# Kernel tuning notes

Measured on AMD Instinct MI355X. Metric: run time of the kernel, lower is better.

The kernel has to match this reference:

```python
import math
import jax, jax.numpy as jnp
import numpy as np

B, T, D = 4, 4096, 512


def setup_inputs() -> dict:
    key = jax.random.key(0)
    k1, _ = jax.random.split(key)
    x = jax.random.normal(k1, (B, T, D), dtype=jnp.float32)
    log_alpha = jnp.zeros((), dtype=jnp.float32)
    return {"x": x, "log_alpha": log_alpha}


def _gelu_tanh(x):
    c = math.sqrt(2.0 / math.pi)
    return 0.5 * x * (1.0 + jnp.tanh(c * (x + 0.044715 * x * x * x)))


def reference(x, log_alpha):
    Bx, Tx, Dx = x.shape
    alpha = jax.nn.softplus(log_alpha)
    # F.normalize(dim=-1): x / max(||x||, eps)
    norm = jnp.maximum(jnp.linalg.norm(x, axis=-1, keepdims=True), 1e-12)
    x_norm = x / norm
    sim = jnp.einsum("btd,bsd->bts", x_norm, x_norm)  # [B,T,T]
    # causal mask: triu incl. diagonal (col >= row) filled with -2.0
    row = jnp.arange(Tx)[:, None]
    col = jnp.arange(Tx)[None, :]
    mask = col >= row  # [T,T]
    sim = jnp.where(mask[None], jnp.float32(-2.0), sim)
    max_sim = jnp.max(sim, axis=-1)  # [B,T]
    max_sim = jnp.maximum(max_sim, -1.0)
    familiarity = (max_sim + 1.0) * 0.5
    novelty = 1.0 - familiarity
    gate = 1.0 + alpha * novelty[..., None]  # [B,T,1]
    return _gelu_tanh(x * gate)
```

## Files before the change

### kernel.cpp

```cpp
#include <hip/hip_runtime.h>
#include <hip/hip_bf16.h>
#include <math.h>

#define B_ 4
#define T_ 4096
#define D_ 512
#define BT 128
#define BK 64
#define STEPS (D_ / BK)
#define NT (T_ / BT)
#define NPAIR (NT * (NT + 1) / 2)


typedef float f32x4 __attribute__((ext_vector_type(4)));
typedef long i64x2 __attribute__((ext_vector_type(2)));

__device__ __forceinline__ unsigned f2ord(float f) {
    unsigned u = __float_as_uint(f);
    return (u & 0x80000000u) ? ~u : (u | 0x80000000u);
}
__device__ __forceinline__ float ord2f(unsigned u) {
    unsigned b = (u & 0x80000000u) ? (u ^ 0x80000000u) : ~u;
    return __uint_as_float(b);
}

__device__ __forceinline__ void async16(const unsigned char* g, unsigned char* l) {
    __builtin_amdgcn_global_load_lds(
        (const __attribute__((address_space(1))) unsigned int*)g,
        (__attribute__((address_space(3))) unsigned int*)l, 16, 0, 0);
}

__global__ __launch_bounds__(256) void k_norm(const float* __restrict__ x,
                                              unsigned char* __restrict__ xn,
                                              unsigned* __restrict__ maxsim) {
    int w = (blockIdx.x * 256 + threadIdx.x) >> 6;
    int l = threadIdx.x & 63;
    const float4* xr = (const float4*)(x + (size_t)w * D_);
    float4 a = xr[l];
    float4 b = xr[l + 64];
    float ss = a.x * a.x + a.y * a.y + a.z * a.z + a.w * a.w +
               b.x * b.x + b.y * b.y + b.z * b.z + b.w * b.w;
#pragma unroll
    for (int off = 32; off > 0; off >>= 1) ss += __shfl_xor(ss, off);
    float inv = 1.0f / fmaxf(sqrtf(ss), 1e-12f);
    int u0 = __builtin_amdgcn_cvt_pk_fp8_f32(a.x * inv, a.y * inv, 0, false);
    u0 = __builtin_amdgcn_cvt_pk_fp8_f32(a.z * inv, a.w * inv, u0, true);
    int u1 = __builtin_amdgcn_cvt_pk_fp8_f32(b.x * inv, b.y * inv, 0, false);
    u1 = __builtin_amdgcn_cvt_pk_fp8_f32(b.z * inv, b.w * inv, u1, true);
    unsigned* xo = (unsigned*)(xn + (size_t)w * D_);
    int off4 = (l >> 4) * 16 + ((l >> 1) & 3) * 4 + ((l >> 3) & 1) * 2 + (l & 1);
    xo[off4]      = (unsigned)u0;
    xo[off4 + 64] = (unsigned)u1;
    if (l == 0) maxsim[w] = f2ord(-2.0f);
}

__global__ __launch_bounds__(256) void k_maxsim(const unsigned char* __restrict__ xn,
                                                unsigned* __restrict__ maxsim) {
    __shared__ __align__(16) unsigned char Buf[3][16384];
    const int b = blockIdx.y;
    const int p = blockIdx.x;
    int ti = (int)((sqrtf(8.0f * (float)p + 1.0f) - 1.0f) * 0.5f);
    while ((ti + 1) * (ti + 2) / 2 <= p) ti++;
    while (ti * (ti + 1) / 2 > p) ti--;
    const int si = p - ti * (ti + 1) / 2;
    const int t0 = ti * BT, s0 = si * BT;

    const int tid = threadIdx.x;
    const int wave = tid >> 6, lane = tid & 63;
    const int wm = wave >> 1, wn = wave & 1;
    const int qa = lane >> 4, la = lane & 15;
    const int swz = (la >> 1) & 3;

    const unsigned char* Ab = xn + (size_t)(b * T_ + t0) * D_;
    const unsigned char* Bb = xn + (size_t)(b * T_ + s0) * D_;

    const int c0 = tid,       r0_ = c0 >> 2, g0 = (c0 & 3) ^ ((r0_ >> 1) & 3);
    const int c1 = 256 + tid, r1_ = c1 >> 2, g1 = (c1 & 3) ^ ((r1_ >> 1) & 3);
    const unsigned char* gA0 = Ab + (size_t)r0_ * D_ + g0 * 16;
    const unsigned char* gA1 = Ab + (size_t)r1_ * D_ + g1 * 16;
    const unsigned char* gB0 = Bb + (size_t)r0_ * D_ + g0 * 16;
    const unsigned char* gB1 = Bb + (size_t)r1_ * D_ + g1 * 16;
    const int ldsb0 = (wave * 64) * 16;
    const int ldsb1 = (256 + wave * 64) * 16;

#define STAGE(step, st)                                            \
    do {                                                           \
        async16(gA0 + (step) * BK, &Buf[st][ldsb0]);               \
        async16(gB0 + (step) * BK, &Buf[st][8192 + ldsb0]);        \
        async16(gA1 + (step) * BK, &Buf[st][ldsb1]);               \
        async16(gB1 + (step) * BK, &Buf[st][8192 + ldsb1]);        \
    } while (0)

    f32x4 acc[4][4];
#pragma unroll
    for (int i = 0; i < 4; i++)
#pragma unroll
        for (int j = 0; j < 4; j++) acc[i][j] = (f32x4){0.f, 0.f, 0.f, 0.f};

    const int rpos = (qa ^ swz) * 16;

    STAGE(0, 0);
    STAGE(1, 1);

#pragma unroll
    for (int k = 0; k < STEPS; ++k) {
        const int cur = k % 3;
        if (k == STEPS - 1) __builtin_amdgcn_s_waitcnt(0x0F70);
        else                __builtin_amdgcn_s_waitcnt(0x0F74);
        __builtin_amdgcn_s_barrier();
        __asm__ __volatile__("" ::: "memory");
        if (k + 2 < STEPS) STAGE(k + 2, (k + 2) % 3);

        const unsigned char* As = &Buf[cur][0];
        const unsigned char* Bs = &Buf[cur][8192];
        i64x2 af[4], bfr[4];
#pragma unroll
        for (int i = 0; i < 4; i++)
            af[i] = *(const i64x2*)&As[(wm * 64 + i * 16 + la) * 64 + rpos];
#pragma unroll
        for (int j = 0; j < 4; j++)
            bfr[j] = *(const i64x2*)&Bs[(wn * 64 + j * 16 + la) * 64 + rpos];
#pragma unroll
        for (int h = 0; h < 2; h++)
#pragma unroll
            for (int i = 0; i < 4; i++)
#pragma unroll
                for (int j = 0; j < 4; j++)
                    acc[i][j] = __builtin_amdgcn_mfma_f32_16x16x32_fp8_fp8(
                        af[i][h], bfr[j][h], acc[i][j], 0, 0, 0);
    }
#undef STAGE

    const bool diag = (ti == si);
#pragma unroll
    for (int i = 0; i < 4; i++) {
#pragma unroll
        for (int r = 0; r < 4; r++) {
            int tl = wm * 64 + i * 16 + qa * 4 + r;
            float m = -2.0f;
#pragma unroll
            for (int j = 0; j < 4; j++) {
                int sl = wn * 64 + j * 16 + la;
                float v = acc[i][j][r];
                if (!diag || sl < tl) m = fmaxf(m, v);
            }
#pragma unroll
            for (int off = 1; off < 16; off <<= 1) m = fmaxf(m, __shfl_xor(m, off));
            if (la == 0) atomicMax(&maxsim[b * T_ + t0 + tl], f2ord(m));
        }
    }
}

__device__ __forceinline__ float gelu_tanh(float y) {
    float t = tanhf(0.7978845608028654f * (y + 0.044715f * y * y * y));
    return 0.5f * y * (1.0f + t);
}

__global__ __launch_bounds__(256) void k_gate(const float* __restrict__ x,
                                              const float* __restrict__ log_alpha,
                                              const unsigned* __restrict__ maxsim,
                                              float* __restrict__ out) {
    int idx = blockIdx.x * 256 + threadIdx.x;
    float la = log_alpha[0];
    float alpha = (la > 20.0f) ? la : log1pf(expf(la));
    int row = idx >> 7;
    float m = fmaxf(ord2f(maxsim[row]), -1.0f);
    float novelty = 1.0f - (m + 1.0f) * 0.5f;
    float gate = 1.0f + alpha * novelty;
    float4 v = ((const float4*)x)[idx];
    float4 o;
    o.x = gelu_tanh(v.x * gate);
    o.y = gelu_tanh(v.y * gate);
    o.z = gelu_tanh(v.z * gate);
    o.w = gelu_tanh(v.w * gate);
    ((float4*)out)[idx] = o;
}

extern "C" void kernel_launch(void* const* d_in, const int* in_sizes, int n_in,
                              void* d_out, int out_size, void* d_ws, size_t ws_size,
                              hipStream_t stream) {
    const float* x = (const float*)d_in[0];
    const float* log_alpha = (const float*)d_in[1];
    float* out = (float*)d_out;

    unsigned* maxsim = (unsigned*)d_ws;
    unsigned char* xn = (unsigned char*)d_ws + 65536;

    const int rows = B_ * T_;
    k_norm<<<rows / 4, 256, 0, stream>>>(x, xn, maxsim);

    dim3 g2(NPAIR, B_);
    k_maxsim<<<g2, 256, 0, stream>>>(xn, maxsim);

    k_gate<<<(B_ * T_ * D_ / 4) / 256, 256, 0, stream>>>(x, log_alpha, maxsim, out);
}
```

Measured before the change: 131.3 us.

## Switch maxsim GEMM to 32x32x64 scaled FP8 MFMA with block-order remap

Replaces the 16x16x32 FP8 MFMA tiles with the gfx950 scaled 32x32x64 f8f6f4 MFMA and unit scales. This cuts the instruction count and the number of LDS fragment loads per K step. It drops the custom byte permutation in the normalization store and changes the LDS read addressing to match the new operand layout. It also remaps block indices so consecutive blocks are strided across the work list, likely to spread work across XCDs for better L2 locality. The new fragment layout and epilogue row mapping add correctness risk.

```diff
diff --git a/kernel.cpp b/kernel.cpp
--- a/kernel.cpp
+++ b/kernel.cpp
@@ -10,10 +10,13 @@
 #define STEPS (D_ / BK)
 #define NT (T_ / BT)
 #define NPAIR (NT * (NT + 1) / 2)
-
-
-typedef float f32x4 __attribute__((ext_vector_type(4)));
-typedef long i64x2 __attribute__((ext_vector_type(2)));
+#define NBLK (NPAIR * B_)
+#define SCL 0x7F7F7F7F
+
+
+typedef float f32x16 __attribute__((ext_vector_type(16)));
+typedef int v4i __attribute__((ext_vector_type(4)));
+typedef int v8i __attribute__((ext_vector_type(8)));
 
 __device__ __forceinline__ unsigned f2ord(float f) {
     unsigned u = __float_as_uint(f);
@@ -48,17 +51,18 @@
     int u1 = __builtin_amdgcn_cvt_pk_fp8_f32(b.x * inv, b.y * inv, 0, false);
     u1 = __builtin_amdgcn_cvt_pk_fp8_f32(b.z * inv, b.w * inv, u1, true);
     unsigned* xo = (unsigned*)(xn + (size_t)w * D_);
-    int off4 = (l >> 4) * 16 + ((l >> 1) & 3) * 4 + ((l >> 3) & 1) * 2 + (l & 1);
-    xo[off4]      = (unsigned)u0;
-    xo[off4 + 64] = (unsigned)u1;
+    xo[l]      = (unsigned)u0;
+    xo[l + 64] = (unsigned)u1;
     if (l == 0) maxsim[w] = f2ord(-2.0f);
 }
 
 __global__ __launch_bounds__(256) void k_maxsim(const unsigned char* __restrict__ xn,
                                                 unsigned* __restrict__ maxsim) {
     __shared__ __align__(16) unsigned char Buf[3][16384];
-    const int b = blockIdx.y;
-    const int p = blockIdx.x;
+    const int lin = blockIdx.x + NPAIR * blockIdx.y;
+    const int wrk = (lin & 7) * (NBLK / 8) + (lin >> 3);
+    const int b = wrk / NPAIR;
+    const int p = wrk - b * NPAIR;
     int ti = (int)((sqrtf(8.0f * (float)p + 1.0f) - 1.0f) * 0.5f);
     while ((ti + 1) * (ti + 2) / 2 <= p) ti++;
     while (ti * (ti + 1) / 2 > p) ti--;
@@ -68,8 +72,8 @@
     const int tid = threadIdx.x;
     const int wave = tid >> 6, lane = tid & 63;
     const int wm = wave >> 1, wn = wave & 1;
-    const int qa = lane >> 4, la = lane & 15;
-    const int swz = (la >> 1) & 3;
+    const int lr = lane & 31;
+    const int h  = lane >> 5;
 
     const unsigned char* Ab = xn + (size_t)(b * T_ + t0) * D_;
     const unsigned char* Bb = xn + (size_t)(b * T_ + s0) * D_;
@@ -91,13 +95,21 @@
         async16(gB1 + (step) * BK, &Buf[st][8192 + ldsb1]);        \
     } while (0)
 
-    f32x4 acc[4][4];
-#pragma unroll
-    for (int i = 0; i < 4; i++)
-#pragma unroll
-        for (int j = 0; j < 4; j++) acc[i][j] = (f32x4){0.f, 0.f, 0.f, 0.f};
-
-    const int rpos = (qa ^ swz) * 16;
+#define MFMA(Aop, Bop, C) \
+    __builtin_amdgcn_mfma_scale_f32_32x32x64_f8f6f4((Aop), (Bop), (C), 0, 0, 0, SCL, 0, SCL)
+
+    f32x16 acc[2][2];
+#pragma unroll
+    for (int i = 0; i < 2; i++)
+#pragma unroll
+        for (int j = 0; j < 2; j++)
+#pragma unroll
+            for (int r = 0; r < 16; r++) acc[i][j][r] = 0.0f;
+
+    const int s_ = (lr >> 1) & 3;
+    const int pb = ((2 * h) ^ s_) * 16;
+    const int offA = (wm * 64 + lr) * 64 + pb;
+    const int offB = 8192 + (wn * 64 + lr) * 64 + pb;
 
     STAGE(0, 0);
     STAGE(1, 1);
@@ -111,42 +123,45 @@
         __asm__ __volatile__("" ::: "memory");
         if (k + 2 < STEPS) STAGE(k + 2, (k + 2) % 3);
 
-        const unsigned char* As = &Buf[cur][0];
-        const unsigned char* Bs = &Buf[cur][8192];
-        i64x2 af[4], bfr[4];
-#pragma unroll
-        for (int i = 0; i < 4; i++)
-            af[i] = *(const i64x2*)&As[(wm * 64 + i * 16 + la) * 64 + rpos];
-#pragma unroll
-        for (int j = 0; j < 4; j++)
-            bfr[j] = *(const i64x2*)&Bs[(wn * 64 + j * 16 + la) * 64 + rpos];
-#pragma unroll
-        for (int h = 0; h < 2; h++)
-#pragma unroll
-            for (int i = 0; i < 4; i++)
-#pragma unroll
-                for (int j = 0; j < 4; j++)
-                    acc[i][j] = __builtin_amdgcn_mfma_f32_16x16x32_fp8_fp8(
-                        af[i][h], bfr[j][h], acc[i][j], 0, 0, 0);
+        const unsigned char* Bs = &Buf[cur][0];
+        v4i a0l = *(const v4i*)(Bs + offA);
+        v4i a0h = *(const v4i*)(Bs + (offA ^ 16));
+        v4i a1l = *(const v4i*)(Bs + offA + 2048);
+        v4i a1h = *(const v4i*)(Bs + (offA ^ 16) + 2048);
+        v4i b0l = *(const v4i*)(Bs + offB);
+        v4i b0h = *(const v4i*)(Bs + (offB ^ 16));
+        v4i b1l = *(const v4i*)(Bs + offB + 2048);
+        v4i b1h = *(const v4i*)(Bs + (offB ^ 16) + 2048);
+        const v8i A0 = __builtin_shufflevector(a0l, a0h, 0, 1, 2, 3, 4, 5, 6, 7);
+        const v8i A1 = __builtin_shufflevector(a1l, a1h, 0, 1, 2, 3, 4, 5, 6, 7);
+        const v8i B0 = __builtin_shufflevector(b0l, b0h, 0, 1, 2, 3, 4, 5, 6, 7);
+        const v8i B1 = __builtin_shufflevector(b1l, b1h, 0, 1, 2, 3, 4, 5, 6, 7);
+        acc[0][0] = MFMA(A0, B0, acc[0][0]);
+        acc[0][1] = MFMA(A0, B1, acc[0][1]);
+        acc[1][0] = MFMA(A1, B0, acc[1][0]);
+        acc[1][1] = MFMA(A1, B1, acc[1][1]);
     }
 #undef STAGE
+#undef MFMA
 
     const bool diag = (ti == si);
 #pragma unroll
-    for (int i = 0; i < 4; i++) {
-#pragma unroll
-        for (int r = 0; r < 4; r++) {
-            int tl = wm * 64 + i * 16 + qa * 4 + r;
+    for (int i = 0; i < 2; i++) {
+#pragma unroll
+        for (int reg = 0; reg < 16; reg++) {
+            const int tl = wm * 64 + i * 32 + (reg & 3) + 8 * (reg >> 2) + 4 * h;
             float m = -2.0f;
-#pragma unroll
-            for (int j = 0; j < 4; j++) {
-                int sl = wn * 64 + j * 16 + la;
-                float v = acc[i][j][r];
-                if (!diag || sl < tl) m = fmaxf(m, v);
+            {
+                const int sl0 = wn * 64 + lr;
+                float v0 = acc[i][0][reg];
+                if (!diag || sl0 < tl) m = fmaxf(m, v0);
+                const int sl1 = sl0 + 32;
+                float v1 = acc[i][1][reg];
+                if (!diag || sl1 < tl) m = fmaxf(m, v1);
             }
 #pragma unroll
-            for (int off = 1; off < 16; off <<= 1) m = fmaxf(m, __shfl_xor(m, off));
-            if (la == 0) atomicMax(&maxsim[b * T_ + t0 + tl], f2ord(m));
+            for (int off = 1; off < 32; off <<= 1) m = fmaxf(m, __shfl_xor(m, off));
+            if (lr == 0) atomicMax(&maxsim[b * T_ + t0 + tl], f2ord(m));
         }
     }
 }
```

After: 220.5 us. +68.0%, slower.

## Process two tile pairs per block with a continuous cross-tile load pipeline

Applied to the files above, without the earlier changes.

Each maxsim block now handles two consecutive (b, tile-pair) work items over 16 K-steps. The triple-buffered async LDS prefetch runs straight through the boundary between them, so the second tile's loads start during the first tile's compute. The first epilogue runs mid-loop at step 8. This halves the block count and removes one pipeline prologue and drain per tile. In exchange there is less parallelism (1056 blocks), a mid-loop epilogue that may stall the MFMA stream, and extra register pressure from holding two sets of coordinates.

```diff
diff --git a/kernel.cpp b/kernel.cpp
--- a/kernel.cpp
+++ b/kernel.cpp
@@ -10,6 +10,7 @@
 #define STEPS (D_ / BK)
 #define NT (T_ / BT)
 #define NPAIR (NT * (NT + 1) / 2)
+#define NBLK (NPAIR * B_)
 
 
 typedef float f32x4 __attribute__((ext_vector_type(4)));
@@ -57,13 +58,6 @@
 __global__ __launch_bounds__(256) void k_maxsim(const unsigned char* __restrict__ xn,
                                                 unsigned* __restrict__ maxsim) {
     __shared__ __align__(16) unsigned char Buf[3][16384];
-    const int b = blockIdx.y;
-    const int p = blockIdx.x;
-    int ti = (int)((sqrtf(8.0f * (float)p + 1.0f) - 1.0f) * 0.5f);
-    while ((ti + 1) * (ti + 2) / 2 <= p) ti++;
-    while (ti * (ti + 1) / 2 > p) ti--;
-    const int si = p - ti * (ti + 1) / 2;
-    const int t0 = ti * BT, s0 = si * BT;
 
     const int tid = threadIdx.x;
     const int wave = tid >> 6, lane = tid & 63;
@@ -71,24 +65,40 @@
     const int qa = lane >> 4, la = lane & 15;
     const int swz = (la >> 1) & 3;
 
-    const unsigned char* Ab = xn + (size_t)(b * T_ + t0) * D_;
-    const unsigned char* Bb = xn + (size_t)(b * T_ + s0) * D_;
-
     const int c0 = tid,       r0_ = c0 >> 2, g0 = (c0 & 3) ^ ((r0_ >> 1) & 3);
     const int c1 = 256 + tid, r1_ = c1 >> 2, g1 = (c1 & 3) ^ ((r1_ >> 1) & 3);
-    const unsigned char* gA0 = Ab + (size_t)r0_ * D_ + g0 * 16;
-    const unsigned char* gA1 = Ab + (size_t)r1_ * D_ + g1 * 16;
-    const unsigned char* gB0 = Bb + (size_t)r0_ * D_ + g0 * 16;
-    const unsigned char* gB1 = Bb + (size_t)r1_ * D_ + g1 * 16;
+    const size_t gofA0 = (size_t)r0_ * D_ + g0 * 16;
+    const size_t gofA1 = (size_t)r1_ * D_ + g1 * 16;
     const int ldsb0 = (wave * 64) * 16;
     const int ldsb1 = (256 + wave * 64) * 16;
 
-#define STAGE(step, st)                                            \
-    do {                                                           \
-        async16(gA0 + (step) * BK, &Buf[st][ldsb0]);               \
-        async16(gB0 + (step) * BK, &Buf[st][8192 + ldsb0]);        \
-        async16(gA1 + (step) * BK, &Buf[st][ldsb1]);               \
-        async16(gB1 + (step) * BK, &Buf[st][8192 + ldsb1]);        \
+    int bb[2], tt0[2], ss0[2];
+    bool dg[2];
+#pragma unroll
+    for (int q = 0; q < 2; q++) {
+        int w = blockIdx.x * 2 + q;
+        int b = w / NPAIR;
+        int p = w - b * NPAIR;
+        int ti = (int)((sqrtf(8.0f * (float)p + 1.0f) - 1.0f) * 0.5f);
+        while ((ti + 1) * (ti + 2) / 2 <= p) ti++;
+        while (ti * (ti + 1) / 2 > p) ti--;
+        int si = p - ti * (ti + 1) / 2;
+        bb[q] = b; tt0[q] = ti * BT; ss0[q] = si * BT; dg[q] = (ti == si);
+    }
+    const unsigned char* pA_0 = xn + (size_t)(bb[0] * T_ + tt0[0]) * D_;
+    const unsigned char* pB_0 = xn + (size_t)(bb[0] * T_ + ss0[0]) * D_;
+    const unsigned char* pA_1 = xn + (size_t)(bb[1] * T_ + tt0[1]) * D_;
+    const unsigned char* pB_1 = xn + (size_t)(bb[1] * T_ + ss0[1]) * D_;
+
+#define STAGE(g)                                                          \
+    do {                                                                  \
+        const unsigned char* _A = ((g) < 8) ? pA_0 : pA_1;                \
+        const unsigned char* _B = ((g) < 8) ? pB_0 : pB_1;                \
+        const int _o = ((g) & 7) * BK;                                    \
+        async16(_A + gofA0 + _o, &Buf[(g) % 3][ldsb0]);                   \
+        async16(_B + gofA0 + _o, &Buf[(g) % 3][8192 + ldsb0]);            \
+        async16(_A + gofA1 + _o, &Buf[(g) % 3][ldsb1]);                   \
+        async16(_B + gofA1 + _o, &Buf[(g) % 3][8192 + ldsb1]);            \
     } while (0)
 
     f32x4 acc[4][4];
@@ -97,19 +107,47 @@
 #pragma unroll
         for (int j = 0; j < 4; j++) acc[i][j] = (f32x4){0.f, 0.f, 0.f, 0.f};
 
+    auto epi = [&](int be, int t0e, bool diage) {
+#pragma unroll
+        for (int i = 0; i < 4; i++) {
+#pragma unroll
+            for (int r = 0; r < 4; r++) {
+                int tl = wm * 64 + i * 16 + qa * 4 + r;
+                float m = -2.0f;
+#pragma unroll
+                for (int j = 0; j < 4; j++) {
+                    int sl = wn * 64 + j * 16 + la;
+                    float v = acc[i][j][r];
+                    if (!diage || sl < tl) m = fmaxf(m, v);
+                }
+#pragma unroll
+                for (int off = 1; off < 16; off <<= 1) m = fmaxf(m, __shfl_xor(m, off));
+                if (la == 0) atomicMax(&maxsim[be * T_ + t0e + tl], f2ord(m));
+            }
+        }
+    };
+
     const int rpos = (qa ^ swz) * 16;
 
-    STAGE(0, 0);
-    STAGE(1, 1);
-
-#pragma unroll
-    for (int k = 0; k < STEPS; ++k) {
+    STAGE(0);
+    STAGE(1);
+
+#pragma unroll
+    for (int k = 0; k < 16; ++k) {
         const int cur = k % 3;
-        if (k == STEPS - 1) __builtin_amdgcn_s_waitcnt(0x0F70);
-        else                __builtin_amdgcn_s_waitcnt(0x0F74);
+        if (k == 15) __builtin_amdgcn_s_waitcnt(0x0F70);
+        else         __builtin_amdgcn_s_waitcnt(0x0F74);
         __builtin_amdgcn_s_barrier();
         __asm__ __volatile__("" ::: "memory");
-        if (k + 2 < STEPS) STAGE(k + 2, (k + 2) % 3);
+        if (k + 2 < 16) STAGE(k + 2);
+
+        if (k == 8) {
+            epi(bb[0], tt0[0], dg[0]);
+#pragma unroll
+            for (int i = 0; i < 4; i++)
+#pragma unroll
+                for (int j = 0; j < 4; j++) acc[i][j] = (f32x4){0.f, 0.f, 0.f, 0.f};
+        }
 
         const unsigned char* As = &Buf[cur][0];
         const unsigned char* Bs = &Buf[cur][8192];
@@ -131,24 +169,7 @@
     }
 #undef STAGE
 
-    const bool diag = (ti == si);
-#pragma unroll
-    for (int i = 0; i < 4; i++) {
-#pragma unroll
-        for (int r = 0; r < 4; r++) {
-            int tl = wm * 64 + i * 16 + qa * 4 + r;
-            float m = -2.0f;
-#pragma unroll
-            for (int j = 0; j < 4; j++) {
-                int sl = wn * 64 + j * 16 + la;
-                float v = acc[i][j][r];
-                if (!diag || sl < tl) m = fmaxf(m, v);
-            }
-#pragma unroll
-            for (int off = 1; off < 16; off <<= 1) m = fmaxf(m, __shfl_xor(m, off));
-            if (la == 0) atomicMax(&maxsim[b * T_ + t0 + tl], f2ord(m));
-        }
-    }
+    epi(bb[1], tt0[1], dg[1]);
 }
 
 __device__ __forceinline__ float gelu_tanh(float y) {
@@ -189,8 +210,7 @@
     const int rows = B_ * T_;
     k_norm<<<rows / 4, 256, 0, stream>>>(x, xn, maxsim);
 
-    dim3 g2(NPAIR, B_);
-    k_maxsim<<<g2, 256, 0, stream>>>(xn, maxsim);
+    k_maxsim<<<NBLK / 2, 256, 0, stream>>>(xn, maxsim);
 
     k_gate<<<(B_ * T_ * D_ / 4) / 256, 256, 0, stream>>>(x, log_alpha, maxsim, out);
 }
```

After: 134.6 us. 2.5% more time.

## Give each wave private LDS staging to drop block barriers in maxsim GEMM

Applied to the files above, without the earlier changes.

Each wave now loads its own 64-row A and B slices into a private double-buffered LDS region instead of sharing a block-wide triple buffer. The per-step s_barrier is removed and replaced by a wait on the wave's own LDS reads before it reuses the buffer. This is meant to remove cross-wave synchronisation stalls. In exchange, tiles that were shared across waves are now loaded twice, so global/L2 traffic rises, and LDS use grows to 64KB, which can lower occupancy.

```diff
diff --git a/kernel.cpp b/kernel.cpp
--- a/kernel.cpp
+++ b/kernel.cpp
@@ -56,7 +56,7 @@
 
 __global__ __launch_bounds__(256) void k_maxsim(const unsigned char* __restrict__ xn,
                                                 unsigned* __restrict__ maxsim) {
-    __shared__ __align__(16) unsigned char Buf[3][16384];
+    __shared__ __align__(16) unsigned char Buf[4][2][8192];
     const int b = blockIdx.y;
     const int p = blockIdx.x;
     int ti = (int)((sqrtf(8.0f * (float)p + 1.0f) - 1.0f) * 0.5f);
@@ -71,24 +71,26 @@
     const int qa = lane >> 4, la = lane & 15;
     const int swz = (la >> 1) & 3;
 
-    const unsigned char* Ab = xn + (size_t)(b * T_ + t0) * D_;
-    const unsigned char* Bb = xn + (size_t)(b * T_ + s0) * D_;
-
-    const int c0 = tid,       r0_ = c0 >> 2, g0 = (c0 & 3) ^ ((r0_ >> 1) & 3);
-    const int c1 = 256 + tid, r1_ = c1 >> 2, g1 = (c1 & 3) ^ ((r1_ >> 1) & 3);
-    const unsigned char* gA0 = Ab + (size_t)r0_ * D_ + g0 * 16;
-    const unsigned char* gA1 = Ab + (size_t)r1_ * D_ + g1 * 16;
-    const unsigned char* gB0 = Bb + (size_t)r0_ * D_ + g0 * 16;
-    const unsigned char* gB1 = Bb + (size_t)r1_ * D_ + g1 * 16;
-    const int ldsb0 = (wave * 64) * 16;
-    const int ldsb1 = (256 + wave * 64) * 16;
-
-#define STAGE(step, st)                                            \
-    do {                                                           \
-        async16(gA0 + (step) * BK, &Buf[st][ldsb0]);               \
-        async16(gB0 + (step) * BK, &Buf[st][8192 + ldsb0]);        \
-        async16(gA1 + (step) * BK, &Buf[st][ldsb1]);               \
-        async16(gB1 + (step) * BK, &Buf[st][8192 + ldsb1]);        \
+    const unsigned char* Ab = xn + (size_t)(b * T_ + t0 + wm * 64) * D_;
+    const unsigned char* Bb = xn + (size_t)(b * T_ + s0 + wn * 64) * D_;
+
+    const int rl = lane >> 2, gl = (lane & 3) ^ ((rl >> 1) & 3);
+    const unsigned char* gAq[4];
+    const unsigned char* gBq[4];
+#pragma unroll
+    for (int q = 0; q < 4; q++) {
+        gAq[q] = Ab + (size_t)(q * 16 + rl) * D_ + gl * 16;
+        gBq[q] = Bb + (size_t)(q * 16 + rl) * D_ + gl * 16;
+    }
+    unsigned char* const lw = &Buf[wave][0][0];
+
+#define STAGE(step, st)                                                  \
+    do {                                                                 \
+        _Pragma("unroll")                                                \
+        for (int q = 0; q < 4; q++) {                                    \
+            async16(gAq[q] + (step) * BK, lw + (st) * 8192 + q * 1024);  \
+            async16(gBq[q] + (step) * BK, lw + (st) * 8192 + 4096 + q * 1024); \
+        }                                                                \
     } while (0)
 
     f32x4 acc[4][4];
@@ -104,22 +106,24 @@
 
 #pragma unroll
     for (int k = 0; k < STEPS; ++k) {
-        const int cur = k % 3;
+        const int cur = k & 1;
         if (k == STEPS - 1) __builtin_amdgcn_s_waitcnt(0x0F70);
-        else                __builtin_amdgcn_s_waitcnt(0x0F74);
-        __builtin_amdgcn_s_barrier();
+        else                __builtin_amdgcn_s_waitcnt(0x0F78);
         __asm__ __volatile__("" ::: "memory");
-        if (k + 2 < STEPS) STAGE(k + 2, (k + 2) % 3);
-
-        const unsigned char* As = &Buf[cur][0];
-        const unsigned char* Bs = &Buf[cur][8192];
+
+        const unsigned char* As = lw + cur * 8192;
+        const unsigned char* Bs = As + 4096;
         i64x2 af[4], bfr[4];
 #pragma unroll
         for (int i = 0; i < 4; i++)
-            af[i] = *(const i64x2*)&As[(wm * 64 + i * 16 + la) * 64 + rpos];
+            af[i] = *(const i64x2*)&As[(i * 16 + la) * 64 + rpos];
 #pragma unroll
         for (int j = 0; j < 4; j++)
-            bfr[j] = *(const i64x2*)&Bs[(wn * 64 + j * 16 + la) * 64 + rpos];
+            bfr[j] = *(const i64x2*)&Bs[(j * 16 + la) * 64 + rpos];
+        __builtin_amdgcn_s_waitcnt(0xC07F);
+        __asm__ __volatile__("" ::: "memory");
+        if (k + 2 < STEPS) STAGE(k + 2, cur);
+
 #pragma unroll
         for (int h = 0; h < 2; h++)
 #pragma unroll
```

New measurement: 143.1 us. +9.0%, slower.
